# Optimization experiments

Hardware: AMD Instinct MI355X
Metric: run time of the kernel (lower is better)

## Reference

```python
import jax, jax.numpy as jnp
import numpy as np
import math


def setup_inputs() -> dict:
    key = jax.random.key(0)
    ks = jax.random.split(key, 10)
    B, N, C, heads = 16, 1024, 256, 8
    nW = 4
    ANGLE_BINS = 5
    inner = C  # dim_head*heads == dim
    return {
        "x": jax.random.normal(ks[0], (B, N, C), jnp.float32),
        "mask": jax.random.normal(ks[1], (nW, N, N), jnp.float32),
        "affine_matrix": jax.random.normal(ks[2], (B, 2, 3), jnp.float32),
        "Wq": jax.random.normal(ks[3], (C, inner), jnp.float32) * (C ** -0.5),
        "bq": jnp.zeros((inner,), jnp.float32),
        "Wkv": jax.random.normal(ks[4], (C, 2 * inner), jnp.float32) * (C ** -0.5),
        "bkv": jnp.zeros((2 * inner,), jnp.float32),
        "Wp": jax.random.normal(ks[5], (C, C), jnp.float32) * (C ** -0.5),
        "bp": jnp.zeros((C,), jnp.float32),
        "angle_table": jnp.ones((ANGLE_BINS, heads), jnp.float32),
        "H": 32,
        "W": 32,
    }


def reference(x, mask, affine_matrix, Wq, bq, Wkv, bkv, Wp, bp, angle_table, H, W):
    B, N, C = x.shape
    heads = angle_table.shape[1]
    hd = C // heads
    scale = hd ** -0.5

    # qkv projections (torch Linear -> x @ W + b with W stored as (in, out))
    q = (x @ Wq + bq).reshape(B, N, heads, hd).transpose(0, 2, 1, 3)      # (B,h,N,d)
    kv = (x @ Wkv + bkv).reshape(B, N, 2, heads, hd).transpose(2, 0, 3, 1, 4)
    k, v = kv[0], kv[1]                                                    # (B,h,N,d)

    attn = jnp.einsum('bhqd,bhkd->bhqk', q * scale, k)                     # (B,h,N,N)

    # angle bias: per-query multiplicative bias in (1,2)
    grid_y, grid_x = jnp.meshgrid(jnp.arange(H), jnp.arange(W), indexing='ij')
    coords = jnp.stack([grid_x.reshape(-1), grid_y.reshape(-1)], -1).astype(jnp.float32)  # (N,2)
    center = jnp.array([W / 2.0, H / 2.0], jnp.float32)
    ego = jnp.einsum('bij,j->bi', affine_matrix[:, :2, :2], center) + affine_matrix[:, :2, 2]  # (B,2)
    rel = coords[None, :, :] - ego[:, None, :]                             # (B,N,2)
    ang = jnp.arctan2(rel[..., 1], rel[..., 0])
    bins = (((ang + math.pi) / (2.0 * math.pi)) * (angle_table.shape[0] - 1)).astype(jnp.int32)
    bias = 1.0 + jax.nn.sigmoid(angle_table[bins])                         # (B,N,h)
    attn = attn * bias.transpose(0, 2, 1)[..., None]                       # broadcast over keys

    # additive window mask then softmax
    nW = mask.shape[0]
    attn = attn.reshape(B // nW, nW, heads, N, N) + mask[None, :, None]
    attn = jax.nn.softmax(attn.reshape(B, heads, N, N), axis=-1)

    out = jnp.einsum('bhqk,bhkd->bhqd', attn, v).transpose(0, 2, 1, 3).reshape(B, N, C)
    return out @ Wp + bp
```

## Files before the change

kernel.cpp:

```cpp
#include <hip/hip_runtime.h>
#include <hip/hip_bf16.h>
#include <math.h>

#define BB 16
#define NTOK 1024
#define CDIM 256
#define HEADS 8
#define HD 32
#define LOG2E 1.4426950408889634f
#define PSHIFT 18.0f

typedef __attribute__((ext_vector_type(8))) _Float16 half8;
typedef __attribute__((ext_vector_type(8))) unsigned short u16x8;
typedef __attribute__((ext_vector_type(4))) unsigned int u32x4;
typedef __attribute__((ext_vector_type(4))) float f32x4;

__device__ __forceinline__ unsigned short f2h(float f) {
  _Float16 h = (_Float16)f;
  return __builtin_bit_cast(unsigned short, h);
}
__device__ __forceinline__ half8 ldh8(const unsigned short* p) {
  return *reinterpret_cast<const half8*>(p);
}
__device__ __forceinline__ void gl_lds16(const void* g, void* l) {
  __builtin_amdgcn_global_load_lds(
      (const __attribute__((address_space(1))) unsigned int*)g,
      (__attribute__((address_space(3))) unsigned int*)l, 16, 0, 0);
}

__global__ __launch_bounds__(256) void cvt_x(const float* __restrict__ X,
                                             unsigned short* __restrict__ x16) {
  size_t base = ((size_t)blockIdx.x * 256 + threadIdx.x) * 8;
  float4 a = *(const float4*)(X + base);
  float4 b = *(const float4*)(X + base + 4);
  u16x8 o = {f2h(a.x), f2h(a.y), f2h(a.z), f2h(a.w),
             f2h(b.x), f2h(b.y), f2h(b.z), f2h(b.w)};
  *(u16x8*)(x16 + base) = o;
}

__global__ __launch_bounds__(256) void cvt_w(
    const float* __restrict__ Wq, const float* __restrict__ Wkv,
    const float* __restrict__ Wp, unsigned short* __restrict__ wt16,
    unsigned short* __restrict__ wp16) {
  int idx = blockIdx.x * 256 + threadIdx.x;
  float val; size_t dst; bool isp = false;
  if (idx < 65536) {
    int k = idx >> 8, n = idx & 255;
    val = Wq[idx]; dst = (size_t)n * 256 + k;
  } else if (idx < 196608) {
    int i2 = idx - 65536;
    int k = i2 >> 9, n2 = i2 & 511;
    val = Wkv[i2]; dst = (size_t)(256 + n2) * 256 + k;
  } else {
    int i3 = idx - 196608;
    int k = i3 >> 8, n = i3 & 255;
    val = Wp[i3]; dst = (size_t)n * 256 + k; isp = true;
  }
  unsigned short h = f2h(val);
  if (isp) wp16[dst] = h; else wt16[dst] = h;
}

__global__ __launch_bounds__(256) void bias_kernel(
    const float* __restrict__ affine, const float* __restrict__ atab,
    float* __restrict__ bias) {
  int idx = blockIdx.x * 256 + threadIdx.x;
  if (idx >= BB * NTOK) return;
  int b = idx >> 10, n = idx & (NTOK - 1);
  float cx = (float)(n & 31);
  float cy = (float)(n >> 5);
  const float* A = affine + b * 6;
  float egx = fmaf(A[0], 16.f, fmaf(A[1], 16.f, A[2]));
  float egy = fmaf(A[3], 16.f, fmaf(A[4], 16.f, A[5]));
  float ang = atan2f(cy - egy, cx - egx);
  float t = (ang + 3.14159265358979323846f) *
            (1.f / (2.f * 3.14159265358979323846f)) * 4.f;
  int bin = (int)t;
  bin = bin < 0 ? 0 : (bin > 4 ? 4 : bin);
  for (int h = 0; h < HEADS; ++h) {
    float a = atab[bin * HEADS + h];
    float s = 1.f / (1.f + __expf(-a));
    bias[((size_t)b * HEADS + h) * NTOK + n] = 1.f + s;
  }
}

__global__ __launch_bounds__(512, 4) void gemm_qkv16(
    const unsigned short* __restrict__ x16, const unsigned short* __restrict__ wt16,
    const float* __restrict__ bq, const float* __restrict__ bkv,
    const float* __restrict__ bias, unsigned short* __restrict__ q16,
    unsigned short* __restrict__ k16, unsigned short* __restrict__ vt16) {
  __shared__ __align__(16) unsigned short SM[16384];
  unsigned short* Xs = SM;
  unsigned short* Ws = SM + 8192;
  int tid = threadIdx.x;
  int w = tid >> 6, l = tid & 63;
  int row16 = l & 15, grp = l >> 4;
  int bid = blockIdx.x;
  int xcd = bid & 7, local = bid >> 3;
  int jb = local % 6, mb = xcd * 16 + local / 6;
  int j0 = jb * 128, m0 = mb * 128;
  int wm = w >> 1, wn = w & 1;

  auto stg = [&](int nb, int kt) {
    int k0s = kt * 32;
    int row = w * 16 + (l >> 2);
    int ge = (((l & 3) * 16) ^ ((row & 3) << 4)) >> 1;
    gl_lds16(x16 + (size_t)(m0 + row) * 256 + k0s + ge, Xs + nb * 4096 + w * 512);
    gl_lds16(wt16 + (size_t)(j0 + row) * 256 + k0s + ge, Ws + nb * 4096 + w * 512);
  };
  auto off16 = [&](int row, int g) {
    return row * 32 + ((((g * 16) ^ ((row & 3) << 4))) >> 1);
  };

  stg(0, 0);
  __syncthreads();

  f32x4 acc[2][4];
#pragma unroll
  for (int i = 0; i < 2; ++i)
#pragma unroll
    for (int c = 0; c < 4; ++c) acc[i][c] = (f32x4){0.f, 0.f, 0.f, 0.f};

  for (int kt = 0; kt < 8; ++kt) {
    int cur = kt & 1;
    if (kt < 7) stg(cur ^ 1, kt + 1);
    half8 a0 = ldh8(Xs + cur * 4096 + off16(wm * 32 + row16, grp));
    half8 a1 = ldh8(Xs + cur * 4096 + off16(wm * 32 + 16 + row16, grp));
#pragma unroll
    for (int c = 0; c < 4; ++c) {
      half8 bh = ldh8(Ws + cur * 4096 + off16(wn * 64 + c * 16 + row16, grp));
      acc[0][c] = __builtin_amdgcn_mfma_f32_16x16x32_f16(a0, bh, acc[0][c], 0, 0, 0);
      acc[1][c] = __builtin_amdgcn_mfma_f32_16x16x32_f16(a1, bh, acc[1][c], 0, 0, 0);
    }
    __syncthreads();
  }

  const float scaleq = 0.17677669529663687f * LOG2E;
  int half_mine = wm >> 1;
  for (int half = 0; half < 2; ++half) {
    if (half_mine == half) {
#pragma unroll
      for (int i = 0; i < 2; ++i) {
#pragma unroll
        for (int c = 0; c < 4; ++c) {
          int col = wn * 64 + c * 16 + row16;
          int jg = j0 + col;
#pragma unroll
          for (int r = 0; r < 4; ++r) {
            int rowl = (wm & 1) * 32 + i * 16 + grp * 4 + r;
            int m = m0 + half * 64 + rowl;
            int b = m >> 10, n = m & (NTOK - 1);
            float val = acc[i][c][r];
            unsigned short o;
            if (jb < 2)
              o = f2h((val + bq[jg]) * scaleq *
                      bias[((size_t)b * HEADS + (jg >> 5)) * NTOK + n]);
            else
              o = f2h(val + bkv[jg - CDIM]);
            SM[rowl * 136 + col] = o;
          }
        }
      }
    }
    __syncthreads();
    if (jb < 4) {
#pragma unroll
      for (int it = 0; it < 2; ++it) {
        int lin = it * 512 + tid;
        int rowb = lin >> 4, oct = lin & 15;
        u16x8 v = *(const u16x8*)&SM[rowb * 136 + oct * 8];
        int m = m0 + half * 64 + rowb;
        int b = m >> 10, n = m & (NTOK - 1);
        int jg = j0 + oct * 8;
        unsigned short* dst; int h, d;
        if (jb < 2) { h = jg >> 5; d = jg & 31; dst = q16; }
        else { int c2 = jg - CDIM; h = c2 >> 5; d = c2 & 31; dst = k16; }
        *(u16x8*)(dst + (((size_t)b * HEADS + h) * NTOK + n) * HD + d) = v;
      }
    } else {
#pragma unroll
      for (int it = 0; it < 2; ++it) {
        int lin = it * 512 + tid;
        int noct = lin >> 7, jl = lin & 127;
        u16x8 v;
#pragma unroll
        for (int e = 0; e < 8; ++e) v[e] = SM[(noct * 8 + e) * 136 + jl];
        int c3 = j0 + jl - 2 * CDIM;
        int h = c3 >> 5, d = c3 & 31;
        int n0 = m0 + half * 64 + noct * 8;
        int b = n0 >> 10, nn = n0 & (NTOK - 1);
        *(u16x8*)(vt16 + (((size_t)b * HEADS + h) * HD + d) * NTOK + nn) = v;
      }
    }
    __syncthreads();
  }
}

__global__ __launch_bounds__(512, 4) void attn16(
    const unsigned short* __restrict__ q16, const unsigned short* __restrict__ k16,
    const unsigned short* __restrict__ vt16, const float* __restrict__ mask,
    unsigned short* __restrict__ ao16) {
  __shared__ __align__(16) unsigned short KT[2][4][1024];
  __shared__ __align__(16) unsigned short VT[2][4][1024];
  __shared__ __align__(16) float MT[2][2048];

  int tid = threadIdx.x;
  int w = tid >> 6, l = tid & 63;
  int row16 = l & 15, grp = l >> 4;
  int bid = blockIdx.x;
  int g = (bid >> 6) * 8 + (bid & 7);
  int inner = (bid >> 3) & 7;
  int qt = g >> 2, b4 = g & 3;
  int brep = inner >> 1, hg = inner & 1;
  int b = brep * 4 + b4;
  int hl = w >> 1, qh = w & 1;
  int head = hg * 4 + hl;
  int bh = b * HEADS + head;
  int q0g = qt * 64;
  int qbase = q0g + qh * 32;

  half8 bq[2];
#pragma unroll
  for (int qb = 0; qb < 2; ++qb)
    bq[qb] = ldh8(q16 + ((size_t)bh * NTOK + qbase + qb * 16 + row16) * HD +
                  grp * 8);

  const float* mbase = mask + (size_t)b4 * NTOK * NTOK;

  f32x4 acc[2][2];
#pragma unroll
  for (int i = 0; i < 2; ++i)
#pragma unroll
    for (int j = 0; j < 2; ++j) acc[i][j] = (f32x4){0.f, 0.f, 0.f, 0.f};
  float lsum[2] = {0.f, 0.f};
  const f32x4 c18 = (f32x4){-PSHIFT, -PSHIFT, -PSHIFT, -PSHIFT};

  auto off32 = [&](int row, int gg) {
    return row * 32 + ((gg ^ ((row >> 1) & 3)) << 3);
  };

  auto stage = [&](int nb, int kt2) {
    int k0n = (kt2 & 31) * 32;
    int key = 2 * (l >> 2) + qh;
    int sk = (l & 3) ^ ((qh * 8 + (l >> 3)) & 3);
    gl_lds16(k16 + ((size_t)bh * NTOK + k0n + key) * HD + sk * 8,
             &KT[nb][hl][qh * 512]);
    int dl = qh * 16 + (l >> 2);
    int sv = (l & 3) ^ ((qh * 8 + (l >> 3)) & 3);
    gl_lds16(vt16 + ((size_t)bh * HD + dl) * NTOK + k0n + sv * 8,
             &VT[nb][hl][qh * 512]);
    int qq = w * 8 + (l >> 3);
    int slot = (l & 7) ^ (qq & 7);
    gl_lds16(mbase + (size_t)(q0g + qq) * NTOK + k0n + slot * 4,
             &MT[nb][w * 256]);
  };

  stage(0, 0);
  __syncthreads();

  for (int kt = 0; kt < 32; ++kt) {
    int cur = kt & 1;
    if (kt < 31) stage(cur ^ 1, kt + 1);

    half8 kf0 = ldh8(&KT[cur][hl][off32(row16, grp)]);
    half8 kf1 = ldh8(&KT[cur][hl][off32(16 + row16, grp)]);
    half8 v0 = ldh8(&VT[cur][hl][off32(row16, grp)]);
    half8 v1 = ldh8(&VT[cur][hl][off32(16 + row16, grp)]);

#pragma unroll
    for (int qb = 0; qb < 2; ++qb) {
      int qr = qh * 32 + qb * 16 + row16;
      int q7 = qr & 7;
      f32x4 mv0 = *(const f32x4*)&MT[cur][cur * 0 + qr * 32 + (((2 * grp) ^ q7) << 2)];
      f32x4 mv1 = *(const f32x4*)&MT[cur][qr * 32 + (((2 * grp + 1) ^ q7) << 2)];
      f32x4 s0 = __builtin_amdgcn_mfma_f32_16x16x32_f16(kf0, bq[qb], c18, 0, 0, 0);
      f32x4 s1 = __builtin_amdgcn_mfma_f32_16x16x32_f16(kf1, bq[qb], c18, 0, 0, 0);
      f32x4 e0, e1;
      e0[0] = __builtin_amdgcn_exp2f(fmaf(mv0[0], LOG2E, s0[0]));
      e1[0] = __builtin_amdgcn_exp2f(fmaf(mv0[1], LOG2E, s1[0]));
      e0[1] = __builtin_amdgcn_exp2f(fmaf(mv0[2], LOG2E, s0[1]));
      e1[1] = __builtin_amdgcn_exp2f(fmaf(mv0[3], LOG2E, s1[1]));
      e0[2] = __builtin_amdgcn_exp2f(fmaf(mv1[0], LOG2E, s0[2]));
      e1[2] = __builtin_amdgcn_exp2f(fmaf(mv1[1], LOG2E, s1[2]));
      e0[3] = __builtin_amdgcn_exp2f(fmaf(mv1[2], LOG2E, s0[3]));
      e1[3] = __builtin_amdgcn_exp2f(fmaf(mv1[3], LOG2E, s1[3]));
      lsum[qb] += ((e0[0] + e1[0]) + (e0[1] + e1[1])) +
                  ((e0[2] + e1[2]) + (e0[3] + e1[3]));
      u32x4 pk;
#pragma unroll
      for (int r = 0; r < 4; ++r)
        pk[r] = __builtin_bit_cast(unsigned,
                                   __builtin_amdgcn_cvt_pkrtz(e0[r], e1[r]));
      half8 pa = __builtin_bit_cast(half8, pk);
      acc[qb][0] = __builtin_amdgcn_mfma_f32_16x16x32_f16(pa, v0, acc[qb][0], 0, 0, 0);
      acc[qb][1] = __builtin_amdgcn_mfma_f32_16x16x32_f16(pa, v1, acc[qb][1], 0, 0, 0);
    }
    __syncthreads();
  }

#pragma unroll
  for (int qb = 0; qb < 2; ++qb) {
    lsum[qb] += __shfl_xor(lsum[qb], 16);
    lsum[qb] += __shfl_xor(lsum[qb], 32);
  }
#pragma unroll
  for (int qb = 0; qb < 2; ++qb) {
#pragma unroll
    for (int r = 0; r < 4; ++r) {
      float lr = __shfl(lsum[qb], grp * 4 + r, 16);
      float inv = 1.f / lr;
      int qrow = qbase + qb * 16 + grp * 4 + r;
      size_t obase = ((size_t)b * NTOK + qrow) * CDIM + head * HD;
      ao16[obase + row16] = f2h(acc[qb][0][r] * inv);
      ao16[obase + 16 + row16] = f2h(acc[qb][1][r] * inv);
    }
  }
}

__global__ __launch_bounds__(512, 4) void gemm_out16(
    const unsigned short* __restrict__ a16, const unsigned short* __restrict__ wp16,
    const float* __restrict__ bp, float* __restrict__ out) {
  __shared__ __align__(16) unsigned short SM[16384];
  unsigned short* Xs = SM;
  unsigned short* Ws = SM + 8192;
  int tid = threadIdx.x;
  int w = tid >> 6, l = tid & 63;
  int row16 = l & 15, grp = l >> 4;
  int bid = blockIdx.x;
  int xcd = bid & 7, local = bid >> 3;
  int jb = local & 1, mb = xcd * 16 + (local >> 1);
  int j0 = jb * 128, m0 = mb * 128;
  int wm = w >> 1, wn = w & 1;

  auto stg = [&](int nb, int kt) {
    int k0s = kt * 32;
    int row = w * 16 + (l >> 2);
    int ge = (((l & 3) * 16) ^ ((row & 3) << 4)) >> 1;
    gl_lds16(a16 + (size_t)(m0 + row) * 256 + k0s + ge, Xs + nb * 4096 + w * 512);
    gl_lds16(wp16 + (size_t)(j0 + row) * 256 + k0s + ge, Ws + nb * 4096 + w * 512);
  };
  auto off16 = [&](int row, int g) {
    return row * 32 + ((((g * 16) ^ ((row & 3) << 4))) >> 1);
  };

  stg(0, 0);
  __syncthreads();

  f32x4 acc[2][4];
#pragma unroll
  for (int i = 0; i < 2; ++i)
#pragma unroll
    for (int c = 0; c < 4; ++c) acc[i][c] = (f32x4){0.f, 0.f, 0.f, 0.f};

  for (int kt = 0; kt < 8; ++kt) {
    int cur = kt & 1;
    if (kt < 7) stg(cur ^ 1, kt + 1);
    half8 a0 = ldh8(Xs + cur * 4096 + off16(wm * 32 + row16, grp));
    half8 a1 = ldh8(Xs + cur * 4096 + off16(wm * 32 + 16 + row16, grp));
#pragma unroll
    for (int c = 0; c < 4; ++c) {
      half8 bh = ldh8(Ws + cur * 4096 + off16(wn * 64 + c * 16 + row16, grp));
      acc[0][c] = __builtin_amdgcn_mfma_f32_16x16x32_f16(a0, bh, acc[0][c], 0, 0, 0);
      acc[1][c] = __builtin_amdgcn_mfma_f32_16x16x32_f16(a1, bh, acc[1][c], 0, 0, 0);
    }
    __syncthreads();
  }

#pragma unroll
  for (int i = 0; i < 2; ++i) {
    int ng = m0 + wm * 32 + i * 16 + grp * 4;
#pragma unroll
    for (int c = 0; c < 4; ++c) {
      int jg = j0 + wn * 64 + c * 16 + row16;
      float bias = bp[jg];
#pragma unroll
      for (int r = 0; r < 4; ++r) {
        out[(size_t)(ng + r) * CDIM + jg] = acc[i][c][r] + bias;
      }
    }
  }
}

extern "C" void kernel_launch(void* const* d_in, const int* in_sizes, int n_in,
                              void* d_out, int out_size, void* d_ws,
                              size_t ws_size, hipStream_t stream) {
  const float* x = (const float*)d_in[0];
  const float* mask = (const float*)d_in[1];
  const float* affine = (const float*)d_in[2];
  const float* Wq = (const float*)d_in[3];
  const float* bq = (const float*)d_in[4];
  const float* Wkv = (const float*)d_in[5];
  const float* bkv = (const float*)d_in[6];
  const float* Wp = (const float*)d_in[7];
  const float* bp = (const float*)d_in[8];
  const float* atab = (const float*)d_in[9];
  float* out = (float*)d_out;

  const size_t bhnd = (size_t)BB * HEADS * NTOK * HD;
  unsigned short* q16 = (unsigned short*)d_ws;
  unsigned short* k16 = q16 + bhnd;
  unsigned short* vt16 = k16 + bhnd;
  unsigned short* x16 = vt16 + bhnd;
  unsigned short* wt16 = x16 + bhnd;
  unsigned short* wp16 = wt16 + 768 * 256;
  float* bias = (float*)(wp16 + 256 * 256);

  cvt_x<<<2048, 256, 0, stream>>>(x, x16);
  cvt_w<<<1024, 256, 0, stream>>>(Wq, Wkv, Wp, wt16, wp16);
  bias_kernel<<<64, 256, 0, stream>>>(affine, atab, bias);
  gemm_qkv16<<<768, 512, 0, stream>>>(x16, wt16, bq, bkv, bias, q16, k16, vt16);
  attn16<<<512, 512, 0, stream>>>(q16, k16, vt16, mask, x16);
  gemm_out16<<<256, 512, 0, stream>>>(x16, wp16, bp, out);
}
```

Measured before the change: 89.87 us.

## Pre-convert mask to swizzled fp16 log2e-scaled slabs and merge prep kernels

The three prep kernels are merged into a single prep_all launch, which also converts the fp32 window mask into fp16, pre-multiplied by log2e and laid out in per-key-tile even/odd slabs that match the attention kernel's fragment layout. The attention kernel now stages half as many mask bytes per tile into LDS and drops the per-element fma with LOG2E. This cuts the repeated fp32 mask reads done by every head-group block and removes launch overhead. In exchange the mask is reduced to fp16, which costs some precision, and the full mask is read and rewritten once more on every call.

New measurement: 87.28 us. 1.03x faster.

```diff
diff --git a/kernel.cpp b/kernel.cpp
--- a/kernel.cpp
+++ b/kernel.cpp
@@ -11,6 +11,7 @@
 #define PSHIFT 18.0f
 
 typedef __attribute__((ext_vector_type(8))) _Float16 half8;
+typedef __attribute__((ext_vector_type(4))) _Float16 half4v;
 typedef __attribute__((ext_vector_type(8))) unsigned short u16x8;
 typedef __attribute__((ext_vector_type(4))) unsigned int u32x4;
 typedef __attribute__((ext_vector_type(4))) float f32x4;
@@ -28,58 +29,76 @@
       (__attribute__((address_space(3))) unsigned int*)l, 16, 0, 0);
 }
 
-__global__ __launch_bounds__(256) void cvt_x(const float* __restrict__ X,
-                                             unsigned short* __restrict__ x16) {
-  size_t base = ((size_t)blockIdx.x * 256 + threadIdx.x) * 8;
-  float4 a = *(const float4*)(X + base);
-  float4 b = *(const float4*)(X + base + 4);
-  u16x8 o = {f2h(a.x), f2h(a.y), f2h(a.z), f2h(a.w),
-             f2h(b.x), f2h(b.y), f2h(b.z), f2h(b.w)};
-  *(u16x8*)(x16 + base) = o;
-}
-
-__global__ __launch_bounds__(256) void cvt_w(
-    const float* __restrict__ Wq, const float* __restrict__ Wkv,
-    const float* __restrict__ Wp, unsigned short* __restrict__ wt16,
-    unsigned short* __restrict__ wp16) {
-  int idx = blockIdx.x * 256 + threadIdx.x;
-  float val; size_t dst; bool isp = false;
-  if (idx < 65536) {
-    int k = idx >> 8, n = idx & 255;
-    val = Wq[idx]; dst = (size_t)n * 256 + k;
-  } else if (idx < 196608) {
-    int i2 = idx - 65536;
-    int k = i2 >> 9, n2 = i2 & 511;
-    val = Wkv[i2]; dst = (size_t)(256 + n2) * 256 + k;
+__global__ __launch_bounds__(256) void prep_all(
+    const float* __restrict__ X, const float* __restrict__ Wq,
+    const float* __restrict__ Wkv, const float* __restrict__ Wp,
+    const float* __restrict__ affine, const float* __restrict__ atab,
+    const float* __restrict__ mask, unsigned short* __restrict__ x16,
+    unsigned short* __restrict__ wt16, unsigned short* __restrict__ wp16,
+    float* __restrict__ bias, unsigned short* __restrict__ mF16) {
+  int bid = blockIdx.x;
+  if (bid < 4096) {
+    int idx = bid * 256 + threadIdx.x;
+    int b4 = idx >> 18;
+    int rem = idx & 262143;
+    int q = rem >> 8;
+    int k = (rem & 255) * 4;
+    float4 v = *(const float4*)(mask + ((size_t)b4 * NTOK + q) * NTOK + k);
+    int kt = k >> 5;
+    int ins0 = (k & 31) >> 1;
+    int gw = (ins0 >> 2) ^ ((q >> 2) & 3);
+    int io = ins0 & 3;
+    size_t off = (size_t)q * 16 + gw * 4 + io;
+    size_t slabE = ((size_t)(b4 * 64 + kt * 2)) * 16384;
+    unsigned eP = (unsigned)f2h(v.x * LOG2E) |
+                  ((unsigned)f2h(v.z * LOG2E) << 16);
+    unsigned oP = (unsigned)f2h(v.y * LOG2E) |
+                  ((unsigned)f2h(v.w * LOG2E) << 16);
+    *(unsigned*)(mF16 + slabE + off) = eP;
+    *(unsigned*)(mF16 + slabE + 16384 + off) = oP;
+  } else if (bid < 6144) {
+    size_t base = ((size_t)(bid - 4096) * 256 + threadIdx.x) * 8;
+    float4 a = *(const float4*)(X + base);
+    float4 b = *(const float4*)(X + base + 4);
+    u16x8 o = {f2h(a.x), f2h(a.y), f2h(a.z), f2h(a.w),
+               f2h(b.x), f2h(b.y), f2h(b.z), f2h(b.w)};
+    *(u16x8*)(x16 + base) = o;
+  } else if (bid < 7168) {
+    int idx = (bid - 6144) * 256 + threadIdx.x;
+    float val; size_t dst; bool isp = false;
+    if (idx < 65536) {
+      int k = idx >> 8, n = idx & 255;
+      val = Wq[idx]; dst = (size_t)n * 256 + k;
+    } else if (idx < 196608) {
+      int i2 = idx - 65536;
+      int k = i2 >> 9, n2 = i2 & 511;
+      val = Wkv[i2]; dst = (size_t)(256 + n2) * 256 + k;
+    } else {
+      int i3 = idx - 196608;
+      int k = i3 >> 8, n = i3 & 255;
+      val = Wp[i3]; dst = (size_t)n * 256 + k; isp = true;
+    }
+    unsigned short h = f2h(val);
+    if (isp) wp16[dst] = h; else wt16[dst] = h;
   } else {
-    int i3 = idx - 196608;
-    int k = i3 >> 8, n = i3 & 255;
-    val = Wp[i3]; dst = (size_t)n * 256 + k; isp = true;
-  }
-  unsigned short h = f2h(val);
-  if (isp) wp16[dst] = h; else wt16[dst] = h;
-}
-
-__global__ __launch_bounds__(256) void bias_kernel(
-    const float* __restrict__ affine, const float* __restrict__ atab,
-    float* __restrict__ bias) {
-  int idx = blockIdx.x * 256 + threadIdx.x;
-  if (idx >= BB * NTOK) return;
-  int b = idx >> 10, n = idx & (NTOK - 1);
-  float cx = (float)(n & 31);
-  float cy = (float)(n >> 5);
-  const float* A = affine + b * 6;
-  float egx = fmaf(A[0], 16.f, fmaf(A[1], 16.f, A[2]));
-  float egy = fmaf(A[3], 16.f, fmaf(A[4], 16.f, A[5]));
-  float ang = atan2f(cy - egy, cx - egx);
-  float t = (ang + 3.14159265358979323846f) *
-            (1.f / (2.f * 3.14159265358979323846f)) * 4.f;
-  int bin = (int)t;
-  bin = bin < 0 ? 0 : (bin > 4 ? 4 : bin);
-  for (int h = 0; h < HEADS; ++h) {
-    float a = atab[bin * HEADS + h];
-    float s = 1.f / (1.f + __expf(-a));
-    bias[((size_t)b * HEADS + h) * NTOK + n] = 1.f + s;
+    int idx = (bid - 7168) * 256 + threadIdx.x;
+    if (idx >= BB * NTOK) return;
+    int b = idx >> 10, n = idx & (NTOK - 1);
+    float cx = (float)(n & 31);
+    float cy = (float)(n >> 5);
+    const float* A = affine + b * 6;
+    float egx = fmaf(A[0], 16.f, fmaf(A[1], 16.f, A[2]));
+    float egy = fmaf(A[3], 16.f, fmaf(A[4], 16.f, A[5]));
+    float ang = atan2f(cy - egy, cx - egx);
+    float t = (ang + 3.14159265358979323846f) *
+              (1.f / (2.f * 3.14159265358979323846f)) * 4.f;
+    int bin = (int)t;
+    bin = bin < 0 ? 0 : (bin > 4 ? 4 : bin);
+    for (int h = 0; h < HEADS; ++h) {
+      float a = atab[bin * HEADS + h];
+      float s = 1.f / (1.f + __expf(-a));
+      bias[((size_t)b * HEADS + h) * NTOK + n] = 1.f + s;
+    }
   }
 }
 
@@ -197,11 +216,11 @@
 
 __global__ __launch_bounds__(512, 4) void attn16(
     const unsigned short* __restrict__ q16, const unsigned short* __restrict__ k16,
-    const unsigned short* __restrict__ vt16, const float* __restrict__ mask,
+    const unsigned short* __restrict__ vt16, const unsigned short* __restrict__ mF16,
     unsigned short* __restrict__ ao16) {
   __shared__ __align__(16) unsigned short KT[2][4][1024];
   __shared__ __align__(16) unsigned short VT[2][4][1024];
-  __shared__ __align__(16) float MT[2][2048];
+  __shared__ __align__(16) unsigned short MT[2][2][1024];
 
   int tid = threadIdx.x;
   int w = tid >> 6, l = tid & 63;
@@ -224,7 +243,7 @@
     bq[qb] = ldh8(q16 + ((size_t)bh * NTOK + qbase + qb * 16 + row16) * HD +
                   grp * 8);
 
-  const float* mbase = mask + (size_t)b4 * NTOK * NTOK;
+  const unsigned short* mFb = mF16 + (size_t)b4 * 64 * 16384;
 
   f32x4 acc[2][2];
 #pragma unroll
@@ -248,10 +267,12 @@
     int sv = (l & 3) ^ ((qh * 8 + (l >> 3)) & 3);
     gl_lds16(vt16 + ((size_t)bh * HD + dl) * NTOK + k0n + sv * 8,
              &VT[nb][hl][qh * 512]);
-    int qq = w * 8 + (l >> 3);
-    int slot = (l & 7) ^ (qq & 7);
-    gl_lds16(mbase + (size_t)(q0g + qq) * NTOK + k0n + slot * 4,
-             &MT[nb][w * 256]);
+    if (w < 4) {
+      int slab = w >> 1, ch = w & 1;
+      gl_lds16(mFb + (size_t)((kt2 & 31) * 2 + slab) * 16384 + q0g * 16 +
+                   ch * 512 + l * 8,
+               &MT[nb][slab][ch * 512]);
+    }
   };
 
   stage(0, 0);
@@ -269,20 +290,17 @@
 #pragma unroll
     for (int qb = 0; qb < 2; ++qb) {
       int qr = qh * 32 + qb * 16 + row16;
-      int q7 = qr & 7;
-      f32x4 mv0 = *(const f32x4*)&MT[cur][cur * 0 + qr * 32 + (((2 * grp) ^ q7) << 2)];
-      f32x4 mv1 = *(const f32x4*)&MT[cur][qr * 32 + (((2 * grp + 1) ^ q7) << 2)];
+      int g2 = grp ^ ((qr >> 2) & 3);
+      half4v me = *(const half4v*)&MT[cur][0][qr * 16 + g2 * 4];
+      half4v mo = *(const half4v*)&MT[cur][1][qr * 16 + g2 * 4];
       f32x4 s0 = __builtin_amdgcn_mfma_f32_16x16x32_f16(kf0, bq[qb], c18, 0, 0, 0);
       f32x4 s1 = __builtin_amdgcn_mfma_f32_16x16x32_f16(kf1, bq[qb], c18, 0, 0, 0);
       f32x4 e0, e1;
-      e0[0] = __builtin_amdgcn_exp2f(fmaf(mv0[0], LOG2E, s0[0]));
-      e1[0] = __builtin_amdgcn_exp2f(fmaf(mv0[1], LOG2E, s1[0]));
-      e0[1] = __builtin_amdgcn_exp2f(fmaf(mv0[2], LOG2E, s0[1]));
-      e1[1] = __builtin_amdgcn_exp2f(fmaf(mv0[3], LOG2E, s1[1]));
-      e0[2] = __builtin_amdgcn_exp2f(fmaf(mv1[0], LOG2E, s0[2]));
-      e1[2] = __builtin_amdgcn_exp2f(fmaf(mv1[1], LOG2E, s1[2]));
-      e0[3] = __builtin_amdgcn_exp2f(fmaf(mv1[2], LOG2E, s0[3]));
-      e1[3] = __builtin_amdgcn_exp2f(fmaf(mv1[3], LOG2E, s1[3]));
+#pragma unroll
+      for (int r = 0; r < 4; ++r) {
+        e0[r] = __builtin_amdgcn_exp2f(s0[r] + (float)me[r]);
+        e1[r] = __builtin_amdgcn_exp2f(s1[r] + (float)mo[r]);
+      }
       lsum[qb] += ((e0[0] + e1[0]) + (e0[1] + e1[1])) +
                   ((e0[2] + e1[2]) + (e0[3] + e1[3]));
       u32x4 pk;
@@ -402,12 +420,12 @@
   unsigned short* x16 = vt16 + bhnd;
   unsigned short* wt16 = x16 + bhnd;
   unsigned short* wp16 = wt16 + 768 * 256;
-  float* bias = (float*)(wp16 + 256 * 256);
-
-  cvt_x<<<2048, 256, 0, stream>>>(x, x16);
-  cvt_w<<<1024, 256, 0, stream>>>(Wq, Wkv, Wp, wt16, wp16);
-  bias_kernel<<<64, 256, 0, stream>>>(affine, atab, bias);
+  unsigned short* mF16 = wp16 + 256 * 256;
+  float* bias = (float*)(mF16 + (size_t)4 * 64 * 16384);
+
+  prep_all<<<7232, 256, 0, stream>>>(x, Wq, Wkv, Wp, affine, atab, mask,
+                                     x16, wt16, wp16, bias, mF16);
   gemm_qkv16<<<768, 512, 0, stream>>>(x16, wt16, bq, bkv, bias, q16, k16, vt16);
-  attn16<<<512, 512, 0, stream>>>(q16, k16, vt16, mask, x16);
+  attn16<<<512, 512, 0, stream>>>(q16, k16, vt16, mF16, x16);
   gemm_out16<<<256, 512, 0, stream>>>(x16, wp16, bp, out);
 }
```
